# Optimization experiments

Measured on AMD Instinct MI355X. Metric: run time of the kernel, lower is better.

Reference implementation:

```python
import jax, jax.numpy as jnp
import numpy as np

N_USERS = 100000
N_ITEMS = 50000
N_ENT = 80000            # items + tags (tags = 30000)
N_NODES = N_USERS + N_ENT
N_EDGES = 800000
D = 64
N_LAYERS = 2


def _center_net(embs, idx, n, W1, b1, W2, b2):
    # CenterIntersection: linear+relu, linear, segment softmax, weighted segment sum
    act = jnp.maximum(embs @ W1.T + b1, 0.0)
    logits = act @ W2.T + b2
    m = jax.ops.segment_max(logits, idx, num_segments=n)
    e = jnp.exp(logits - m[idx])
    s = jax.ops.segment_sum(e, idx, num_segments=n)
    att = e / s[idx]
    return jax.ops.segment_sum(att * embs, idx, num_segments=n)


def _offset_net(embs, idx, mask, n, use_min, W1, b1, W2, b2):
    # BoxOffsetIntersection restricted to edges where mask is True
    mf = mask[:, None].astype(embs.dtype)
    act = jnp.maximum(embs @ W1.T + b1, 0.0) * mf
    cnt = jax.ops.segment_sum(mask.astype(embs.dtype), idx, num_segments=n)
    mean = jax.ops.segment_sum(act, idx, num_segments=n) / jnp.maximum(cnt, 1.0)[:, None]
    gate = jax.nn.sigmoid(mean @ W2.T + b2)
    if use_min:
        src = jnp.where(mask[:, None], embs, jnp.inf)
        red = jax.ops.segment_min(src, idx, num_segments=n)
    else:
        src = jnp.where(mask[:, None], embs, -jnp.inf)
        red = jax.ops.segment_max(src, idx, num_segments=n)
    red = jnp.where(jnp.isfinite(red), red, 0.0)  # torch_scatter fills empty segments with 0
    return red * gate


def setup_inputs() -> dict:
    key = jax.random.key(0)
    ks = jax.random.split(key, 10)
    s = 0.05  # xavier-like scale
    return {
        "user_emb": jax.random.normal(ks[0], (N_USERS, D), jnp.float32),
        "user_offset_emb": jax.random.normal(ks[1], (N_USERS, D), jnp.float32),
        "item_emb": jax.random.normal(ks[2], (N_ENT, D), jnp.float32),
        "item_offset_emb": jax.random.normal(ks[3], (N_ENT, D), jnp.float32),
        "cW1": jax.random.normal(ks[4], (D, D), jnp.float32) * s,
        "cb1": jnp.zeros((D,), jnp.float32),
        "cW2": jax.random.normal(ks[5], (D, D), jnp.float32) * s,
        "cb2": jnp.zeros((D,), jnp.float32),
        "oW1": jax.random.normal(ks[6], (D, D), jnp.float32) * s,
        "ob1": jnp.zeros((D,), jnp.float32),
        "oW2": jax.random.normal(ks[7], (D, D), jnp.float32) * s,
        "ob2": jnp.zeros((D,), jnp.float32),
        "head": jax.random.randint(ks[8], (N_EDGES,), 0, N_NODES, jnp.int32),
        "tail": jax.random.randint(ks[9], (N_EDGES,), 0, N_NODES, jnp.int32),
    }


def reference(user_emb, user_offset_emb, item_emb, item_offset_emb,
              cW1, cb1, cW2, cb2, oW1, ob1, oW2, ob2, head, tail):
    all_embs = jnp.concatenate([user_emb, item_emb], axis=0)              # [N_NODES, D]
    all_off = jnp.maximum(jnp.concatenate([user_offset_emb, item_offset_emb], axis=0), 0.0)
    uu_idx = jnp.concatenate([jnp.arange(N_USERS), jnp.arange(N_USERS)])
    uu_mask = jnp.ones((2 * N_USERS,), bool)
    m_inter = (tail >= N_USERS) & (head < N_USERS) & (tail < N_USERS + N_ITEMS)
    m_ut = (head < N_USERS) & (tail >= N_USERS + N_ITEMS)
    m_item = (head >= N_USERS) & (head < N_USERS + N_ITEMS)
    m_tag = head >= N_USERS + N_ITEMS
    for _ in range(N_LAYERS):
        h_embs = all_embs[tail]                                           # [E, D] gather
        agg_emb = _center_net(h_embs, head, N_NODES, cW1, cb1, cW2, cb2)
        edge_off = jnp.maximum(all_off[tail], 0.0)                        # [E, D]
        inter_u = _offset_net(edge_off, head, m_inter, N_NODES, True, oW1, ob1, oW2, ob2)[:N_USERS]
        ut_u = _offset_net(edge_off, head, m_ut, N_NODES, False, oW1, ob1, oW2, ob2)[:N_USERS]
        item_o = _offset_net(edge_off, head, m_item, N_NODES, False, oW1, ob1, oW2, ob2)[N_USERS:N_USERS + N_ITEMS]
        tag_o = _offset_net(edge_off, head, m_tag, N_NODES, True, oW1, ob1, oW2, ob2)[N_USERS + N_ITEMS:]
        uo_cat = jnp.concatenate([inter_u, ut_u], axis=0)                 # [2*N_USERS, D]
        user_o = jnp.maximum(_offset_net(uo_cat, uu_idx, uu_mask, N_USERS, False, oW1, ob1, oW2, ob2), 0.0)
        agg_off = jnp.concatenate([user_o, item_o, tag_o], axis=0)
        agg_emb = agg_emb / jnp.maximum(jnp.linalg.norm(agg_emb, axis=1, keepdims=True), 1e-12)  # F.normalize
        all_embs = agg_emb
        all_off = agg_off
    return (all_embs[:N_USERS], all_off[:N_USERS], all_embs[N_USERS:], all_off[N_USERS:])
```

## Files before the change

### kernel.cpp

```cpp
#include <hip/hip_runtime.h>
#include <hip/hip_fp16.h>
#include <math.h>

#define NU 100000
#define NI 50000
#define NENT 80000
#define NN 180000
#define NEDGE 800000
#define SCAN_NB ((NN + 1023) / 1024)

typedef _Float16 f16x4 __attribute__((ext_vector_type(4)));
typedef _Float16 f16x2 __attribute__((ext_vector_type(2)));
typedef float f32x4 __attribute__((ext_vector_type(4)));

__device__ __forceinline__ float sigmoid_f(float x) { return 1.0f / (1.0f + __expf(-x)); }
__device__ __forceinline__ unsigned pack2(float a, float b) {
    __half2 h = __floats2half2_rn(a, b);
    return *(unsigned*)&h;
}
__device__ __forceinline__ f16x2 u2h2(unsigned u) { union { unsigned u; f16x2 h; } x; x.u = u; return x.h; }
__device__ __forceinline__ float fdot2f(f16x2 a, f16x2 b, float c) {
#if __has_builtin(__builtin_amdgcn_fdot2)
    return __builtin_amdgcn_fdot2(a, b, c, false);
#else
    return (float)a[0] * (float)b[0] + (float)a[1] * (float)b[1] + c;
#endif
}
__device__ __forceinline__ _Float16 hminf(_Float16 a, _Float16 b) { return a < b ? a : b; }
__device__ __forceinline__ _Float16 hmaxf(_Float16 a, _Float16 b) { return a > b ? a : b; }
__device__ __forceinline__ f16x4 frag4(const float* __restrict__ p) {
    float4 v = *(const float4*)p;
    f16x4 r; r[0] = (_Float16)v.x; r[1] = (_Float16)v.y; r[2] = (_Float16)v.z; r[3] = (_Float16)v.w;
    return r;
}
__device__ __forceinline__ f16x4 frag4r(const float* __restrict__ p) {
    float4 v = *(const float4*)p;
    f16x4 r;
    r[0] = (_Float16)fmaxf(v.x, 0.f); r[1] = (_Float16)fmaxf(v.y, 0.f);
    r[2] = (_Float16)fmaxf(v.z, 0.f); r[3] = (_Float16)fmaxf(v.w, 0.f);
    return r;
}
__device__ __forceinline__ f16x4 fragp(const _Float16* __restrict__ Wp, int dt, int ks, int lane) {
    return *(const f16x4*)(Wp + (((dt * 4 + ks) * 64 + lane) << 2));
}
__device__ __forceinline__ f32x4 mm(f16x4 a, f16x4 b, f32x4 c) {
    return __builtin_amdgcn_mfma_f32_16x16x16f16(a, b, c, 0, 0, 0);
}

__global__ __launch_bounds__(256) void prep_w(
    const float* __restrict__ W0, const float* __restrict__ W1,
    const float* __restrict__ W2, const float* __restrict__ W3,
    _Float16* __restrict__ out)
{
    int idx = blockIdx.x * 256 + threadIdx.x;
    int mat = idx >> 12, wi = idx & 4095;
    const float* W = (mat == 0) ? W0 : (mat == 1) ? W1 : (mat == 2) ? W2 : W3;
    int tile = wi >> 8;
    int dt = tile >> 2, ks = tile & 3;
    int ln = (wi >> 2) & 63, j = wi & 3;
    int lr = ln & 15, lk = ln >> 4;
    out[idx] = (_Float16)W[(size_t)(dt * 16 + lr) * 64 + ks * 16 + lk * 4 + j];
}

__global__ __launch_bounds__(256) void node_pass(
    const float* __restrict__ embU, const float* __restrict__ embE,
    const float* __restrict__ offU, const float* __restrict__ offE,
    const _Float16* __restrict__ cW1f, const float* __restrict__ cb1,
    const _Float16* __restrict__ cW2f, const float* __restrict__ cb2,
    const _Float16* __restrict__ oW1f, const float* __restrict__ ob1,
    uint2* __restrict__ packed)
{
    __shared__ _Float16 tb[4][16 * 72];
    int lane = threadIdx.x & 63, wid = threadIdx.x >> 6;
    int n0 = (blockIdx.x * 4 + wid) * 16;
    if (n0 >= NN) return;
    int lr = lane & 15, lk = lane >> 4;
    const float* eb; const float* ob;
    if (n0 < NU) { eb = embU + (size_t)n0 * 64; ob = offU + (size_t)n0 * 64; }
    else         { eb = embE + (size_t)(n0 - NU) * 64; ob = offE + (size_t)(n0 - NU) * 64; }

    f16x4 ax[4];
    #pragma unroll
    for (int ks = 0; ks < 4; ++ks) ax[ks] = frag4(eb + (size_t)lr * 64 + ks * 16 + lk * 4);
    f32x4 acc[4];
    #pragma unroll
    for (int dt = 0; dt < 4; ++dt) {
        float b = cb1[dt * 16 + lr];
        f32x4 c = {b, b, b, b};
        #pragma unroll
        for (int ks = 0; ks < 4; ++ks) c = mm(ax[ks], fragp(cW1f, dt, ks, lane), c);
        acc[dt] = c;
    }
    _Float16* T = tb[wid];
    #pragma unroll
    for (int dt = 0; dt < 4; ++dt)
        #pragma unroll
        for (int r = 0; r < 4; ++r)
            T[(lk * 4 + r) * 72 + dt * 16 + lr] = (_Float16)fmaxf(acc[dt][r], 0.f);
    f16x4 a1[4];
    #pragma unroll
    for (int ks = 0; ks < 4; ++ks) a1[ks] = *(const f16x4*)(T + lr * 72 + ks * 16 + lk * 4);
    #pragma unroll
    for (int dt = 0; dt < 4; ++dt) {
        float b = cb2[dt * 16 + lr];
        f32x4 c = {b, b, b, b};
        #pragma unroll
        for (int ks = 0; ks < 4; ++ks) c = mm(a1[ks], fragp(cW2f, dt, ks, lane), c);
        acc[dt] = c;
    }
    f16x4 axo[4];
    #pragma unroll
    for (int ks = 0; ks < 4; ++ks) axo[ks] = frag4r(ob + (size_t)lr * 64 + ks * 16 + lk * 4);
    f32x4 acco[4];
    #pragma unroll
    for (int dt = 0; dt < 4; ++dt) {
        float b = ob1[dt * 16 + lr];
        f32x4 c = {b, b, b, b};
        #pragma unroll
        for (int ks = 0; ks < 4; ++ks) c = mm(axo[ks], fragp(oW1f, dt, ks, lane), c);
        acco[dt] = c;
    }
    #pragma unroll
    for (int ks = 0; ks < 4; ++ks) *(f16x4*)(T + lr * 72 + ks * 16 + lk * 4) = ax[ks];
    _Float16 xv[16];
    #pragma unroll
    for (int dt = 0; dt < 4; ++dt)
        #pragma unroll
        for (int r = 0; r < 4; ++r) xv[dt * 4 + r] = T[(lk * 4 + r) * 72 + dt * 16 + lr];
    #pragma unroll
    for (int ks = 0; ks < 4; ++ks) *(f16x4*)(T + lr * 72 + ks * 16 + lk * 4) = axo[ks];
    #pragma unroll
    for (int dt = 0; dt < 4; ++dt) {
        #pragma unroll
        for (int r = 0; r < 4; ++r) {
            int li = lk * 4 + r;
            float ev = __expf(acc[dt][r]);
            float xf = (float)xv[dt * 4 + r];
            float ovf = (float)T[(lk * 4 + r) * 72 + dt * 16 + lr];
            float aov = fmaxf(acco[dt][r], 0.f);
            packed[(size_t)(n0 + li) * 64 + dt * 16 + lr] = make_uint2(pack2(ev, ev * xf), pack2(aov, ovf));
        }
    }
}

__global__ __launch_bounds__(256) void hist_k(const int* __restrict__ head, int* __restrict__ counts) {
    int e = blockIdx.x * 256 + threadIdx.x;
    if (e < NEDGE) atomicAdd(&counts[head[e]], 1);
}

__global__ __launch_bounds__(1024) void scan_local(const int* __restrict__ counts,
                                                   int* __restrict__ excl, int* __restrict__ partials) {
    __shared__ int wsum[16];
    int tid = threadIdx.x, lane = tid & 63, wid = tid >> 6;
    int i = blockIdx.x * 1024 + tid;
    int v = (i < NN) ? counts[i] : 0;
    int s = v;
    #pragma unroll
    for (int d = 1; d < 64; d <<= 1) { int u = __shfl_up(s, d, 64); if (lane >= d) s += u; }
    if (lane == 63) wsum[wid] = s;
    __syncthreads();
    if (wid == 0 && lane < 16) {
        int w = wsum[lane];
        #pragma unroll
        for (int d = 1; d < 16; d <<= 1) { int u = __shfl_up(w, d, 64); if (lane >= d) w += u; }
        wsum[lane] = w;
    }
    __syncthreads();
    int base = wid ? wsum[wid - 1] : 0;
    if (i < NN) excl[i] = base + s - v;
    if (tid == 1023) partials[blockIdx.x] = wsum[15];
}

__global__ __launch_bounds__(256) void scan_carry(const int* __restrict__ partials, int* __restrict__ carries) {
    __shared__ int ws[4];
    int tid = threadIdx.x, lane = tid & 63, wid = tid >> 6;
    int v = (tid < SCAN_NB) ? partials[tid] : 0;
    int s = v;
    #pragma unroll
    for (int d = 1; d < 64; d <<= 1) { int u = __shfl_up(s, d, 64); if (lane >= d) s += u; }
    if (lane == 63) ws[wid] = s;
    __syncthreads();
    int add = 0;
    for (int w = 0; w < wid; ++w) add += ws[w];
    if (tid < SCAN_NB) carries[tid] = add + s - v;
}

__global__ __launch_bounds__(1024) void scan_add(int* __restrict__ excl, const int* __restrict__ carries,
                                                 int* __restrict__ cursor) {
    int i = blockIdx.x * 1024 + threadIdx.x;
    if (i < NN) { int o = excl[i] + carries[blockIdx.x]; excl[i] = o; cursor[i] = o; }
    if (i == 0) excl[NN] = NEDGE;
}

__global__ __launch_bounds__(256) void scatter_k(const int* __restrict__ head, const int* __restrict__ tail,
                                                 int* __restrict__ cursor, int* __restrict__ sorted_t) {
    int e = blockIdx.x * 256 + threadIdx.x;
    if (e < NEDGE) { int pos = atomicAdd(&cursor[head[e]], 1); sorted_t[pos] = tail[e]; }
}

__global__ __launch_bounds__(256) void seg_pass(
    const uint2* __restrict__ packed,
    const int* __restrict__ offsets, const int* __restrict__ sorted_t,
    float* __restrict__ embOutU, float* __restrict__ embOutE,
    _Float16* __restrict__ meanI, _Float16* __restrict__ redI,
    _Float16* __restrict__ meanU, _Float16* __restrict__ redU,
    _Float16* __restrict__ meanE, _Float16* __restrict__ redE)
{
    int lane = threadIdx.x & 63;
    int h = blockIdx.x * 4 + (threadIdx.x >> 6);
    int beg = offsets[h], end = offsets[h + 1];
    bool isUser = (h < NU);
    bool entMin = (h >= NU + NI);
    const f16x2 SEL_LO = {(_Float16)1.0f, (_Float16)0.0f};
    const f16x2 SEL_HI = {(_Float16)0.0f, (_Float16)1.0f};
    float num = 0.f, den = 0.f, s_i = 0.f, s_u = 0.f;
    const _Float16 HINF = u2h2(0x7C007C00u)[0];
    _Float16 m_i = (isUser || entMin) ? HINF : (_Float16)0.f;
    _Float16 m_u = (_Float16)0.f;
    int c_i = 0, c_u = 0;

    const char* pbase = (const char*)packed;
    int loff = lane << 3;
    for (int base = beg; base < end; base += 64) {
        int rem = end - base; if (rem > 64) rem = 64;
        int tv = sorted_t[base + (lane < rem ? lane : 0)];
        int t0 = __builtin_amdgcn_readlane(tv, 0);
        uint2 q0 = *(const uint2*)(pbase + ((size_t)(unsigned)t0 << 9) + loff);
        int t1 = t0; uint2 q1 = q0;
        if (rem > 1) {
            t1 = __builtin_amdgcn_readlane(tv, 1);
            q1 = *(const uint2*)(pbase + ((size_t)(unsigned)t1 << 9) + loff);
        }
        for (int j = 0; j < rem; ++j) {
            int tc = t0; uint2 qc = q0;
            t0 = t1; q0 = q1;
            if (j + 2 < rem) {
                t1 = __builtin_amdgcn_readlane(tv, j + 2);
                q1 = *(const uint2*)(pbase + ((size_t)(unsigned)t1 << 9) + loff);
            }
            f16x2 evp = u2h2(qc.x);
            den = fdot2f(evp, SEL_LO, den);
            num = fdot2f(evp, SEL_HI, num);
            f16x2 aoo = u2h2(qc.y);
            if (isUser) {
                if (tc >= NU) {
                    if (tc < NU + NI) { s_i = fdot2f(aoo, SEL_LO, s_i); m_i = hminf(m_i, aoo[1]); c_i++; }
                    else              { s_u = fdot2f(aoo, SEL_LO, s_u); m_u = hmaxf(m_u, aoo[1]); c_u++; }
                }
            } else {
                s_i = fdot2f(aoo, SEL_LO, s_i); c_i++;
                m_i = entMin ? hminf(m_i, aoo[1]) : hmaxf(m_i, aoo[1]);
            }
        }
    }
    float v = (den > 0.f) ? num / den : 0.f;
    float sq = v * v;
    #pragma unroll
    for (int m = 32; m; m >>= 1) sq += __shfl_xor(sq, m, 64);
    v = v / fmaxf(sqrtf(sq), 1e-12f);

    float m_if = (float)m_i;
    if (m_if > 1e37f) m_if = 0.f;
    float rc_i = __builtin_amdgcn_rcpf(fmaxf((float)c_i, 1.f));
    if (isUser) {
        embOutU[(size_t)h * 64 + lane] = v;
        size_t r = (size_t)h * 64 + lane;
        float rc_u = __builtin_amdgcn_rcpf(fmaxf((float)c_u, 1.f));
        meanI[r] = (_Float16)(s_i * rc_i);
        redI[r]  = (_Float16)m_if;
        meanU[r] = (_Float16)(s_u * rc_u);
        redU[r]  = m_u;
    } else {
        embOutE[(size_t)(h - NU) * 64 + lane] = v;
        size_t r = (size_t)(h - NU) * 64 + lane;
        meanE[r] = (_Float16)(s_i * rc_i);
        redE[r]  = (_Float16)m_if;
    }
}

__global__ __launch_bounds__(256) void ent_fin(
    const _Float16* __restrict__ meanE, const _Float16* __restrict__ redE,
    const _Float16* __restrict__ oW2f, const float* __restrict__ ob2,
    float* __restrict__ entOff)
{
    int lane = threadIdx.x & 63, wid = threadIdx.x >> 6;
    int n0 = (blockIdx.x * 4 + wid) * 16;
    if (n0 >= NENT) return;
    int lr = lane & 15, lk = lane >> 4;
    f16x4 am[4];
    #pragma unroll
    for (int ks = 0; ks < 4; ++ks) am[ks] = *(const f16x4*)(meanE + (size_t)(n0 + lr) * 64 + ks * 16 + lk * 4);
    #pragma unroll
    for (int dt = 0; dt < 4; ++dt) {
        float b = ob2[dt * 16 + lr];
        f32x4 c = {b, b, b, b};
        #pragma unroll
        for (int ks = 0; ks < 4; ++ks) c = mm(am[ks], fragp(oW2f, dt, ks, lane), c);
        #pragma unroll
        for (int r = 0; r < 4; ++r) {
            size_t row = (size_t)(n0 + lk * 4 + r);
            entOff[row * 64 + dt * 16 + lr] = (float)redE[row * 64 + dt * 16 + lr] * sigmoid_f(c[r]);
        }
    }
}

__global__ __launch_bounds__(256) void user_fin2(
    const _Float16* __restrict__ meanI, const _Float16* __restrict__ redI,
    const _Float16* __restrict__ meanU, const _Float16* __restrict__ redU,
    const _Float16* __restrict__ oW1f, const float* __restrict__ ob1,
    const _Float16* __restrict__ oW2f, const float* __restrict__ ob2,
    float* __restrict__ outOffU)
{
    __shared__ _Float16 tb[4][16 * 72];
    int lane = threadIdx.x & 63, wid = threadIdx.x >> 6;
    int u0 = (blockIdx.x * 4 + wid) * 16;
    if (u0 >= NU) return;
    int lr = lane & 15, lk = lane >> 4;
    _Float16* T = tb[wid];

    f16x4 W1f[4][4], W2f[4][4];
    float b1d[4], b2d[4];
    #pragma unroll
    for (int dt = 0; dt < 4; ++dt) {
        b1d[dt] = ob1[dt * 16 + lr]; b2d[dt] = ob2[dt * 16 + lr];
        #pragma unroll
        for (int ks = 0; ks < 4; ++ks) {
            W1f[dt][ks] = fragp(oW1f, dt, ks, lane);
            W2f[dt][ks] = fragp(oW2f, dt, ks, lane);
        }
    }

    f16x4 am[4];
    #pragma unroll
    for (int ks = 0; ks < 4; ++ks) am[ks] = *(const f16x4*)(meanI + (size_t)(u0 + lr) * 64 + ks * 16 + lk * 4);
    f32x4 iu[4], uu[4];
    #pragma unroll
    for (int dt = 0; dt < 4; ++dt) {
        f32x4 c = {b2d[dt], b2d[dt], b2d[dt], b2d[dt]};
        #pragma unroll
        for (int ks = 0; ks < 4; ++ks) c = mm(am[ks], W2f[dt][ks], c);
        #pragma unroll
        for (int r = 0; r < 4; ++r)
            iu[dt][r] = (float)redI[(size_t)(u0 + lk * 4 + r) * 64 + dt * 16 + lr] * sigmoid_f(c[r]);
    }
    #pragma unroll
    for (int ks = 0; ks < 4; ++ks) am[ks] = *(const f16x4*)(meanU + (size_t)(u0 + lr) * 64 + ks * 16 + lk * 4);
    #pragma unroll
    for (int dt = 0; dt < 4; ++dt) {
        f32x4 c = {b2d[dt], b2d[dt], b2d[dt], b2d[dt]};
        #pragma unroll
        for (int ks = 0; ks < 4; ++ks) c = mm(am[ks], W2f[dt][ks], c);
        #pragma unroll
        for (int r = 0; r < 4; ++r)
            uu[dt][r] = (float)redU[(size_t)(u0 + lk * 4 + r) * 64 + dt * 16 + lr] * sigmoid_f(c[r]);
    }
    #pragma unroll
    for (int dt = 0; dt < 4; ++dt)
        #pragma unroll
        for (int r = 0; r < 4; ++r) T[(lk * 4 + r) * 72 + dt * 16 + lr] = (_Float16)iu[dt][r];
    #pragma unroll
    for (int ks = 0; ks < 4; ++ks) am[ks] = *(const f16x4*)(T + lr * 72 + ks * 16 + lk * 4);
    f32x4 mn[4];
    #pragma unroll
    for (int dt = 0; dt < 4; ++dt) {
        f32x4 c = {b1d[dt], b1d[dt], b1d[dt], b1d[dt]};
        #pragma unroll
        for (int ks = 0; ks < 4; ++ks) c = mm(am[ks], W1f[dt][ks], c);
        #pragma unroll
        for (int r = 0; r < 4; ++r) mn[dt][r] = fmaxf(c[r], 0.f);
    }
    #pragma unroll
    for (int dt = 0; dt < 4; ++dt)
        #pragma unroll
        for (int r = 0; r < 4; ++r) T[(lk * 4 + r) * 72 + dt * 16 + lr] = (_Float16)uu[dt][r];
    #pragma unroll
    for (int ks = 0; ks < 4; ++ks) am[ks] = *(const f16x4*)(T + lr * 72 + ks * 16 + lk * 4);
    #pragma unroll
    for (int dt = 0; dt < 4; ++dt) {
        f32x4 c = {b1d[dt], b1d[dt], b1d[dt], b1d[dt]};
        #pragma unroll
        for (int ks = 0; ks < 4; ++ks) c = mm(am[ks], W1f[dt][ks], c);
        #pragma unroll
        for (int r = 0; r < 4; ++r) mn[dt][r] = 0.5f * (mn[dt][r] + fmaxf(c[r], 0.f));
    }
    #pragma unroll
    for (int dt = 0; dt < 4; ++dt)
        #pragma unroll
        for (int r = 0; r < 4; ++r) T[(lk * 4 + r) * 72 + dt * 16 + lr] = (_Float16)mn[dt][r];
    #pragma unroll
    for (int ks = 0; ks < 4; ++ks) am[ks] = *(const f16x4*)(T + lr * 72 + ks * 16 + lk * 4);
    #pragma unroll
    for (int dt = 0; dt < 4; ++dt) {
        f32x4 c = {b2d[dt], b2d[dt], b2d[dt], b2d[dt]};
        #pragma unroll
        for (int ks = 0; ks < 4; ++ks) c = mm(am[ks], W2f[dt][ks], c);
        #pragma unroll
        for (int r = 0; r < 4; ++r)
            outOffU[(size_t)(u0 + lk * 4 + r) * 64 + dt * 16 + lr] =
                fmaxf(fmaxf(iu[dt][r], uu[dt][r]) * sigmoid_f(c[r]), 0.f);
    }
}

extern "C" void kernel_launch(void* const* d_in, const int* in_sizes, int n_in,
                              void* d_out, int out_size, void* d_ws, size_t ws_size,
                              hipStream_t stream)
{
    const float* user_emb = (const float*)d_in[0];
    const float* user_off = (const float*)d_in[1];
    const float* item_emb = (const float*)d_in[2];
    const float* item_off = (const float*)d_in[3];
    const float* cW1 = (const float*)d_in[4];
    const float* cb1 = (const float*)d_in[5];
    const float* cW2 = (const float*)d_in[6];
    const float* cb2 = (const float*)d_in[7];
    const float* oW1 = (const float*)d_in[8];
    const float* ob1 = (const float*)d_in[9];
    const float* oW2 = (const float*)d_in[10];
    const float* ob2 = (const float*)d_in[11];
    const int* head = (const int*)d_in[12];
    const int* tail = (const int*)d_in[13];
    float* out = (float*)d_out;

    float* ws = (float*)d_ws;
    const size_t SZ = (size_t)NN * 64;
    float* A      = ws;
    float* B      = A + SZ;
    uint2* packed = (uint2*)(B + SZ);
    _Float16* meanI_h = (_Float16*)(packed + SZ);
    _Float16* redI_h  = meanI_h + (size_t)NU * 64;
    _Float16* meanU_h = redI_h + (size_t)NU * 64;
    _Float16* redU_h  = meanU_h + (size_t)NU * 64;
    _Float16* meanE_h = redU_h + (size_t)NU * 64;
    _Float16* redE_h  = meanE_h + (size_t)NENT * 64;
    _Float16* wpre    = redE_h + (size_t)NENT * 64;
    int* counts   = (int*)(wpre + 4 * 4096);
    int* offsets  = counts + NN;
    int* cursor   = offsets + NN + 1;
    int* sorted_t = cursor + NN;
    int* partials = sorted_t + NEDGE;
    int* carries  = partials + SCAN_NB;

    const _Float16* cW1f = wpre;
    const _Float16* cW2f = wpre + 4096;
    const _Float16* oW1f = wpre + 8192;
    const _Float16* oW2f = wpre + 12288;

    prep_w<<<64, 256, 0, stream>>>(cW1, cW2, oW1, oW2, wpre);
    hipMemsetAsync(counts, 0, NN * sizeof(int), stream);
    hist_k<<<(NEDGE + 255) / 256, 256, 0, stream>>>(head, counts);
    scan_local<<<SCAN_NB, 1024, 0, stream>>>(counts, offsets, partials);
    scan_carry<<<1, 256, 0, stream>>>(partials, carries);
    scan_add<<<SCAN_NB, 1024, 0, stream>>>(offsets, carries, cursor);
    scatter_k<<<(NEDGE + 255) / 256, 256, 0, stream>>>(head, tail, cursor, sorted_t);

    for (int layer = 0; layer < 2; ++layer) {
        const float *eU, *eE, *oU, *oE;
        float *embOutU, *embOutE, *entOff, *uOffOut;
        if (layer == 0) {
            eU = user_emb; eE = item_emb; oU = user_off; oE = item_off;
            embOutU = A;               embOutE = A + (size_t)NU * 64;
            entOff  = B + (size_t)NU * 64;
            uOffOut = B;
        } else {
            eU = A; eE = A + (size_t)NU * 64; oU = B; oE = B + (size_t)NU * 64;
            embOutU = out;             embOutE = out + (size_t)2 * NU * 64;
            entOff  = out + ((size_t)2 * NU + NENT) * 64;
            uOffOut = out + (size_t)NU * 64;
        }
        node_pass<<<(NN + 63) / 64, 256, 0, stream>>>(eU, eE, oU, oE,
                                                      cW1f, cb1, cW2f, cb2, oW1f, ob1, packed);
        seg_pass<<<NN / 4, 256, 0, stream>>>(packed, offsets, sorted_t,
                                             embOutU, embOutE,
                                             meanI_h, redI_h, meanU_h, redU_h,
                                             meanE_h, redE_h);
        ent_fin<<<(NENT / 16 + 3) / 4, 256, 0, stream>>>(meanE_h, redE_h, oW2f, ob2, entOff);
        user_fin2<<<(NU + 63) / 64, 256, 0, stream>>>(meanI_h, redI_h, meanU_h, redU_h,
                                                      oW1f, ob1, oW2f, ob2, uOffOut);
    }
}
```

Measured before the change: 444.5 us.

## Store layer-1 intermediates in fp16 and split packed edge data into two arrays

Layer-1 embeddings and offsets are now written to and read from the workspace as fp16 instead of fp32, which halves the traffic between the two layers. The packed per-node payload is split into separate softmax and offset arrays. In seg_pass, user segments then load the offset half only for neighbours that are entities, so neighbours that are users skip the second load. The cost is one extra fp16 rounding of the intermediate embeddings and two narrower gathers in place of one 8-byte gather.

```diff
diff --git a/kernel.cpp b/kernel.cpp
--- a/kernel.cpp
+++ b/kernel.cpp
@@ -28,17 +28,31 @@
 }
 __device__ __forceinline__ _Float16 hminf(_Float16 a, _Float16 b) { return a < b ? a : b; }
 __device__ __forceinline__ _Float16 hmaxf(_Float16 a, _Float16 b) { return a > b ? a : b; }
-__device__ __forceinline__ f16x4 frag4(const float* __restrict__ p) {
-    float4 v = *(const float4*)p;
-    f16x4 r; r[0] = (_Float16)v.x; r[1] = (_Float16)v.y; r[2] = (_Float16)v.z; r[3] = (_Float16)v.w;
-    return r;
-}
-__device__ __forceinline__ f16x4 frag4r(const float* __restrict__ p) {
-    float4 v = *(const float4*)p;
-    f16x4 r;
-    r[0] = (_Float16)fmaxf(v.x, 0.f); r[1] = (_Float16)fmaxf(v.y, 0.f);
-    r[2] = (_Float16)fmaxf(v.z, 0.f); r[3] = (_Float16)fmaxf(v.w, 0.f);
-    return r;
+
+template<typename T>
+__device__ __forceinline__ f16x4 ldfrag(const T* __restrict__ p) {
+    if constexpr (sizeof(T) == 2) {
+        return *(const f16x4*)p;
+    } else {
+        float4 v = *(const float4*)p;
+        f16x4 r; r[0] = (_Float16)v.x; r[1] = (_Float16)v.y; r[2] = (_Float16)v.z; r[3] = (_Float16)v.w;
+        return r;
+    }
+}
+template<typename T>
+__device__ __forceinline__ f16x4 ldfragr(const T* __restrict__ p) {
+    if constexpr (sizeof(T) == 2) {
+        f16x4 v = *(const f16x4*)p;
+        #pragma unroll
+        for (int i = 0; i < 4; ++i) v[i] = hmaxf(v[i], (_Float16)0.f);
+        return v;
+    } else {
+        float4 v = *(const float4*)p;
+        f16x4 r;
+        r[0] = (_Float16)fmaxf(v.x, 0.f); r[1] = (_Float16)fmaxf(v.y, 0.f);
+        r[2] = (_Float16)fmaxf(v.z, 0.f); r[3] = (_Float16)fmaxf(v.w, 0.f);
+        return r;
+    }
 }
 __device__ __forceinline__ f16x4 fragp(const _Float16* __restrict__ Wp, int dt, int ks, int lane) {
     return *(const f16x4*)(Wp + (((dt * 4 + ks) * 64 + lane) << 2));
@@ -62,26 +76,27 @@
     out[idx] = (_Float16)W[(size_t)(dt * 16 + lr) * 64 + ks * 16 + lk * 4 + j];
 }
 
+template<typename T>
 __global__ __launch_bounds__(256) void node_pass(
-    const float* __restrict__ embU, const float* __restrict__ embE,
-    const float* __restrict__ offU, const float* __restrict__ offE,
+    const T* __restrict__ embU, const T* __restrict__ embE,
+    const T* __restrict__ offU, const T* __restrict__ offE,
     const _Float16* __restrict__ cW1f, const float* __restrict__ cb1,
     const _Float16* __restrict__ cW2f, const float* __restrict__ cb2,
     const _Float16* __restrict__ oW1f, const float* __restrict__ ob1,
-    uint2* __restrict__ packed)
+    unsigned* __restrict__ packedA, unsigned* __restrict__ packedB)
 {
     __shared__ _Float16 tb[4][16 * 72];
     int lane = threadIdx.x & 63, wid = threadIdx.x >> 6;
     int n0 = (blockIdx.x * 4 + wid) * 16;
     if (n0 >= NN) return;
     int lr = lane & 15, lk = lane >> 4;
-    const float* eb; const float* ob;
+    const T* eb; const T* ob;
     if (n0 < NU) { eb = embU + (size_t)n0 * 64; ob = offU + (size_t)n0 * 64; }
     else         { eb = embE + (size_t)(n0 - NU) * 64; ob = offE + (size_t)(n0 - NU) * 64; }
 
     f16x4 ax[4];
     #pragma unroll
-    for (int ks = 0; ks < 4; ++ks) ax[ks] = frag4(eb + (size_t)lr * 64 + ks * 16 + lk * 4);
+    for (int ks = 0; ks < 4; ++ks) ax[ks] = ldfrag(eb + (size_t)lr * 64 + ks * 16 + lk * 4);
     f32x4 acc[4];
     #pragma unroll
     for (int dt = 0; dt < 4; ++dt) {
@@ -91,15 +106,15 @@
         for (int ks = 0; ks < 4; ++ks) c = mm(ax[ks], fragp(cW1f, dt, ks, lane), c);
         acc[dt] = c;
     }
-    _Float16* T = tb[wid];
+    _Float16* T16 = tb[wid];
     #pragma unroll
     for (int dt = 0; dt < 4; ++dt)
         #pragma unroll
         for (int r = 0; r < 4; ++r)
-            T[(lk * 4 + r) * 72 + dt * 16 + lr] = (_Float16)fmaxf(acc[dt][r], 0.f);
+            T16[(lk * 4 + r) * 72 + dt * 16 + lr] = (_Float16)fmaxf(acc[dt][r], 0.f);
     f16x4 a1[4];
     #pragma unroll
-    for (int ks = 0; ks < 4; ++ks) a1[ks] = *(const f16x4*)(T + lr * 72 + ks * 16 + lk * 4);
+    for (int ks = 0; ks < 4; ++ks) a1[ks] = *(const f16x4*)(T16 + lr * 72 + ks * 16 + lk * 4);
     #pragma unroll
     for (int dt = 0; dt < 4; ++dt) {
         float b = cb2[dt * 16 + lr];
@@ -110,7 +125,7 @@
     }
     f16x4 axo[4];
     #pragma unroll
-    for (int ks = 0; ks < 4; ++ks) axo[ks] = frag4r(ob + (size_t)lr * 64 + ks * 16 + lk * 4);
+    for (int ks = 0; ks < 4; ++ks) axo[ks] = ldfragr(ob + (size_t)lr * 64 + ks * 16 + lk * 4);
     f32x4 acco[4];
     #pragma unroll
     for (int dt = 0; dt < 4; ++dt) {
@@ -121,14 +136,14 @@
         acco[dt] = c;
     }
     #pragma unroll
-    for (int ks = 0; ks < 4; ++ks) *(f16x4*)(T + lr * 72 + ks * 16 + lk * 4) = ax[ks];
+    for (int ks = 0; ks < 4; ++ks) *(f16x4*)(T16 + lr * 72 + ks * 16 + lk * 4) = ax[ks];
     _Float16 xv[16];
     #pragma unroll
     for (int dt = 0; dt < 4; ++dt)
         #pragma unroll
-        for (int r = 0; r < 4; ++r) xv[dt * 4 + r] = T[(lk * 4 + r) * 72 + dt * 16 + lr];
-    #pragma unroll
-    for (int ks = 0; ks < 4; ++ks) *(f16x4*)(T + lr * 72 + ks * 16 + lk * 4) = axo[ks];
+        for (int r = 0; r < 4; ++r) xv[dt * 4 + r] = T16[(lk * 4 + r) * 72 + dt * 16 + lr];
+    #pragma unroll
+    for (int ks = 0; ks < 4; ++ks) *(f16x4*)(T16 + lr * 72 + ks * 16 + lk * 4) = axo[ks];
     #pragma unroll
     for (int dt = 0; dt < 4; ++dt) {
         #pragma unroll
@@ -136,9 +151,11 @@
             int li = lk * 4 + r;
             float ev = __expf(acc[dt][r]);
             float xf = (float)xv[dt * 4 + r];
-            float ovf = (float)T[(lk * 4 + r) * 72 + dt * 16 + lr];
+            float ovf = (float)T16[(lk * 4 + r) * 72 + dt * 16 + lr];
             float aov = fmaxf(acco[dt][r], 0.f);
-            packed[(size_t)(n0 + li) * 64 + dt * 16 + lr] = make_uint2(pack2(ev, ev * xf), pack2(aov, ovf));
+            size_t idx = (size_t)(n0 + li) * 64 + dt * 16 + lr;
+            packedA[idx] = pack2(ev, ev * xf);
+            packedB[idx] = pack2(aov, ovf);
         }
     }
 }
@@ -198,10 +215,11 @@
     if (e < NEDGE) { int pos = atomicAdd(&cursor[head[e]], 1); sorted_t[pos] = tail[e]; }
 }
 
+template<bool OUT16>
 __global__ __launch_bounds__(256) void seg_pass(
-    const uint2* __restrict__ packed,
+    const unsigned* __restrict__ packedA, const unsigned* __restrict__ packedB,
     const int* __restrict__ offsets, const int* __restrict__ sorted_t,
-    float* __restrict__ embOutU, float* __restrict__ embOutE,
+    void* __restrict__ embOutU_, void* __restrict__ embOutE_,
     _Float16* __restrict__ meanI, _Float16* __restrict__ redI,
     _Float16* __restrict__ meanU, _Float16* __restrict__ redU,
     _Float16* __restrict__ meanE, _Float16* __restrict__ redE)
@@ -219,37 +237,43 @@
     _Float16 m_u = (_Float16)0.f;
     int c_i = 0, c_u = 0;
 
-    const char* pbase = (const char*)packed;
-    int loff = lane << 3;
+    const char* pA = (const char*)packedA;
+    const char* pB = (const char*)packedB;
+    int loff = lane << 2;
     for (int base = beg; base < end; base += 64) {
         int rem = end - base; if (rem > 64) rem = 64;
         int tv = sorted_t[base + (lane < rem ? lane : 0)];
         int t0 = __builtin_amdgcn_readlane(tv, 0);
-        uint2 q0 = *(const uint2*)(pbase + ((size_t)(unsigned)t0 << 9) + loff);
-        int t1 = t0; uint2 q1 = q0;
+        unsigned a0 = *(const unsigned*)(pA + ((size_t)(unsigned)t0 << 8) + loff);
+        unsigned b0 = 0;
+        if (!isUser || t0 >= NU) b0 = *(const unsigned*)(pB + ((size_t)(unsigned)t0 << 8) + loff);
+        int t1 = t0; unsigned a1 = a0, b1 = b0;
         if (rem > 1) {
             t1 = __builtin_amdgcn_readlane(tv, 1);
-            q1 = *(const uint2*)(pbase + ((size_t)(unsigned)t1 << 9) + loff);
+            a1 = *(const unsigned*)(pA + ((size_t)(unsigned)t1 << 8) + loff);
+            if (!isUser || t1 >= NU) b1 = *(const unsigned*)(pB + ((size_t)(unsigned)t1 << 8) + loff);
         }
         for (int j = 0; j < rem; ++j) {
-            int tc = t0; uint2 qc = q0;
-            t0 = t1; q0 = q1;
+            int tc = t0; unsigned qa = a0, qb = b0;
+            t0 = t1; a0 = a1; b0 = b1;
             if (j + 2 < rem) {
                 t1 = __builtin_amdgcn_readlane(tv, j + 2);
-                q1 = *(const uint2*)(pbase + ((size_t)(unsigned)t1 << 9) + loff);
+                a1 = *(const unsigned*)(pA + ((size_t)(unsigned)t1 << 8) + loff);
+                if (!isUser || t1 >= NU) b1 = *(const unsigned*)(pB + ((size_t)(unsigned)t1 << 8) + loff);
             }
-            f16x2 evp = u2h2(qc.x);
-            den = fdot2f(evp, SEL_LO, den);
-            num = fdot2f(evp, SEL_HI, num);
-            f16x2 aoo = u2h2(qc.y);
+            f16x2 ea = u2h2(qa);
+            den = fdot2f(ea, SEL_LO, den);
+            num = fdot2f(ea, SEL_HI, num);
             if (isUser) {
                 if (tc >= NU) {
-                    if (tc < NU + NI) { s_i = fdot2f(aoo, SEL_LO, s_i); m_i = hminf(m_i, aoo[1]); c_i++; }
-                    else              { s_u = fdot2f(aoo, SEL_LO, s_u); m_u = hmaxf(m_u, aoo[1]); c_u++; }
+                    f16x2 ab = u2h2(qb);
+                    if (tc < NU + NI) { s_i = fdot2f(ab, SEL_LO, s_i); m_i = hminf(m_i, ab[1]); c_i++; }
+                    else              { s_u = fdot2f(ab, SEL_LO, s_u); m_u = hmaxf(m_u, ab[1]); c_u++; }
                 }
             } else {
-                s_i = fdot2f(aoo, SEL_LO, s_i); c_i++;
-                m_i = entMin ? hminf(m_i, aoo[1]) : hmaxf(m_i, aoo[1]);
+                f16x2 ab = u2h2(qb);
+                s_i = fdot2f(ab, SEL_LO, s_i); c_i++;
+                m_i = entMin ? hminf(m_i, ab[1]) : hmaxf(m_i, ab[1]);
             }
         }
     }
@@ -263,25 +287,28 @@
     if (m_if > 1e37f) m_if = 0.f;
     float rc_i = __builtin_amdgcn_rcpf(fmaxf((float)c_i, 1.f));
     if (isUser) {
-        embOutU[(size_t)h * 64 + lane] = v;
         size_t r = (size_t)h * 64 + lane;
+        if constexpr (OUT16) ((_Float16*)embOutU_)[r] = (_Float16)v;
+        else                 ((float*)embOutU_)[r] = v;
         float rc_u = __builtin_amdgcn_rcpf(fmaxf((float)c_u, 1.f));
         meanI[r] = (_Float16)(s_i * rc_i);
         redI[r]  = (_Float16)m_if;
         meanU[r] = (_Float16)(s_u * rc_u);
         redU[r]  = m_u;
     } else {
-        embOutE[(size_t)(h - NU) * 64 + lane] = v;
         size_t r = (size_t)(h - NU) * 64 + lane;
+        if constexpr (OUT16) ((_Float16*)embOutE_)[r] = (_Float16)v;
+        else                 ((float*)embOutE_)[r] = v;
         meanE[r] = (_Float16)(s_i * rc_i);
         redE[r]  = (_Float16)m_if;
     }
 }
 
+template<bool OUT16>
 __global__ __launch_bounds__(256) void ent_fin(
     const _Float16* __restrict__ meanE, const _Float16* __restrict__ redE,
     const _Float16* __restrict__ oW2f, const float* __restrict__ ob2,
-    float* __restrict__ entOff)
+    void* __restrict__ entOff_)
 {
     int lane = threadIdx.x & 63, wid = threadIdx.x >> 6;
     int n0 = (blockIdx.x * 4 + wid) * 16;
@@ -299,24 +326,27 @@
         #pragma unroll
         for (int r = 0; r < 4; ++r) {
             size_t row = (size_t)(n0 + lk * 4 + r);
-            entOff[row * 64 + dt * 16 + lr] = (float)redE[row * 64 + dt * 16 + lr] * sigmoid_f(c[r]);
+            float val = (float)redE[row * 64 + dt * 16 + lr] * sigmoid_f(c[r]);
+            if constexpr (OUT16) ((_Float16*)entOff_)[row * 64 + dt * 16 + lr] = (_Float16)val;
+            else                 ((float*)entOff_)[row * 64 + dt * 16 + lr] = val;
         }
     }
 }
 
+template<bool OUT16>
 __global__ __launch_bounds__(256) void user_fin2(
     const _Float16* __restrict__ meanI, const _Float16* __restrict__ redI,
     const _Float16* __restrict__ meanU, const _Float16* __restrict__ redU,
     const _Float16* __restrict__ oW1f, const float* __restrict__ ob1,
     const _Float16* __restrict__ oW2f, const float* __restrict__ ob2,
-    float* __restrict__ outOffU)
+    void* __restrict__ outOffU_)
 {
     __shared__ _Float16 tb[4][16 * 72];
     int lane = threadIdx.x & 63, wid = threadIdx.x >> 6;
     int u0 = (blockIdx.x * 4 + wid) * 16;
     if (u0 >= NU) return;
     int lr = lane & 15, lk = lane >> 4;
-    _Float16* T = tb[wid];
+    _Float16* T16 = tb[wid];
 
     f16x4 W1f[4][4], W2f[4][4];
     float b1d[4], b2d[4];
@@ -357,9 +387,9 @@
     #pragma unroll
     for (int dt = 0; dt < 4; ++dt)
         #pragma unroll
-        for (int r = 0; r < 4; ++r) T[(lk * 4 + r) * 72 + dt * 16 + lr] = (_Float16)iu[dt][r];
-    #pragma unroll
-    for (int ks = 0; ks < 4; ++ks) am[ks] = *(const f16x4*)(T + lr * 72 + ks * 16 + lk * 4);
+        for (int r = 0; r < 4; ++r) T16[(lk * 4 + r) * 72 + dt * 16 + lr] = (_Float16)iu[dt][r];
+    #pragma unroll
+    for (int ks = 0; ks < 4; ++ks) am[ks] = *(const f16x4*)(T16 + lr * 72 + ks * 16 + lk * 4);
     f32x4 mn[4];
     #pragma unroll
     for (int dt = 0; dt < 4; ++dt) {
@@ -372,9 +402,9 @@
     #pragma unroll
     for (int dt = 0; dt < 4; ++dt)
         #pragma unroll
-        for (int r = 0; r < 4; ++r) T[(lk * 4 + r) * 72 + dt * 16 + lr] = (_Float16)uu[dt][r];
-    #pragma unroll
-    for (int ks = 0; ks < 4; ++ks) am[ks] = *(const f16x4*)(T + lr * 72 + ks * 16 + lk * 4);
+        for (int r = 0; r < 4; ++r) T16[(lk * 4 + r) * 72 + dt * 16 + lr] = (_Float16)uu[dt][r];
+    #pragma unroll
+    for (int ks = 0; ks < 4; ++ks) am[ks] = *(const f16x4*)(T16 + lr * 72 + ks * 16 + lk * 4);
     #pragma unroll
     for (int dt = 0; dt < 4; ++dt) {
         f32x4 c = {b1d[dt], b1d[dt], b1d[dt], b1d[dt]};
@@ -386,18 +416,21 @@
     #pragma unroll
     for (int dt = 0; dt < 4; ++dt)
         #pragma unroll
-        for (int r = 0; r < 4; ++r) T[(lk * 4 + r) * 72 + dt * 16 + lr] = (_Float16)mn[dt][r];
-    #pragma unroll
-    for (int ks = 0; ks < 4; ++ks) am[ks] = *(const f16x4*)(T + lr * 72 + ks * 16 + lk * 4);
+        for (int r = 0; r < 4; ++r) T16[(lk * 4 + r) * 72 + dt * 16 + lr] = (_Float16)mn[dt][r];
+    #pragma unroll
+    for (int ks = 0; ks < 4; ++ks) am[ks] = *(const f16x4*)(T16 + lr * 72 + ks * 16 + lk * 4);
     #pragma unroll
     for (int dt = 0; dt < 4; ++dt) {
         f32x4 c = {b2d[dt], b2d[dt], b2d[dt], b2d[dt]};
         #pragma unroll
         for (int ks = 0; ks < 4; ++ks) c = mm(am[ks], W2f[dt][ks], c);
         #pragma unroll
-        for (int r = 0; r < 4; ++r)
-            outOffU[(size_t)(u0 + lk * 4 + r) * 64 + dt * 16 + lr] =
-                fmaxf(fmaxf(iu[dt][r], uu[dt][r]) * sigmoid_f(c[r]), 0.f);
+        for (int r = 0; r < 4; ++r) {
+            float val = fmaxf(fmaxf(iu[dt][r], uu[dt][r]) * sigmoid_f(c[r]), 0.f);
+            size_t idx = (size_t)(u0 + lk * 4 + r) * 64 + dt * 16 + lr;
+            if constexpr (OUT16) ((_Float16*)outOffU_)[idx] = (_Float16)val;
+            else                 ((float*)outOffU_)[idx] = val;
+        }
     }
 }
 
@@ -421,12 +454,12 @@
     const int* tail = (const int*)d_in[13];
     float* out = (float*)d_out;
 
-    float* ws = (float*)d_ws;
     const size_t SZ = (size_t)NN * 64;
-    float* A      = ws;
-    float* B      = A + SZ;
-    uint2* packed = (uint2*)(B + SZ);
-    _Float16* meanI_h = (_Float16*)(packed + SZ);
+    _Float16* A16   = (_Float16*)d_ws;
+    _Float16* B16   = A16 + SZ;
+    unsigned* packedA = (unsigned*)(B16 + SZ);
+    unsigned* packedB = packedA + SZ;
+    _Float16* meanI_h = (_Float16*)(packedB + SZ);
     _Float16* redI_h  = meanI_h + (size_t)NU * 64;
     _Float16* meanU_h = redI_h + (size_t)NU * 64;
     _Float16* redU_h  = meanU_h + (size_t)NU * 64;
@@ -453,28 +486,27 @@
     scan_add<<<SCAN_NB, 1024, 0, stream>>>(offsets, carries, cursor);
     scatter_k<<<(NEDGE + 255) / 256, 256, 0, stream>>>(head, tail, cursor, sorted_t);
 
-    for (int layer = 0; layer < 2; ++layer) {
-        const float *eU, *eE, *oU, *oE;
-        float *embOutU, *embOutE, *entOff, *uOffOut;
-        if (layer == 0) {
-            eU = user_emb; eE = item_emb; oU = user_off; oE = item_off;
-            embOutU = A;               embOutE = A + (size_t)NU * 64;
-            entOff  = B + (size_t)NU * 64;
-            uOffOut = B;
-        } else {
-            eU = A; eE = A + (size_t)NU * 64; oU = B; oE = B + (size_t)NU * 64;
-            embOutU = out;             embOutE = out + (size_t)2 * NU * 64;
-            entOff  = out + ((size_t)2 * NU + NENT) * 64;
-            uOffOut = out + (size_t)NU * 64;
-        }
-        node_pass<<<(NN + 63) / 64, 256, 0, stream>>>(eU, eE, oU, oE,
-                                                      cW1f, cb1, cW2f, cb2, oW1f, ob1, packed);
-        seg_pass<<<NN / 4, 256, 0, stream>>>(packed, offsets, sorted_t,
-                                             embOutU, embOutE,
-                                             meanI_h, redI_h, meanU_h, redU_h,
-                                             meanE_h, redE_h);
-        ent_fin<<<(NENT / 16 + 3) / 4, 256, 0, stream>>>(meanE_h, redE_h, oW2f, ob2, entOff);
-        user_fin2<<<(NU + 63) / 64, 256, 0, stream>>>(meanI_h, redI_h, meanU_h, redU_h,
-                                                      oW1f, ob1, oW2f, ob2, uOffOut);
-    }
-}
+    node_pass<float><<<(NN + 63) / 64, 256, 0, stream>>>(
+        user_emb, item_emb, user_off, item_off,
+        cW1f, cb1, cW2f, cb2, oW1f, ob1, packedA, packedB);
+    seg_pass<true><<<NN / 4, 256, 0, stream>>>(
+        packedA, packedB, offsets, sorted_t,
+        A16, A16 + (size_t)NU * 64,
+        meanI_h, redI_h, meanU_h, redU_h, meanE_h, redE_h);
+    ent_fin<true><<<(NENT / 16 + 3) / 4, 256, 0, stream>>>(
+        meanE_h, redE_h, oW2f, ob2, B16 + (size_t)NU * 64);
+    user_fin2<true><<<(NU + 63) / 64, 256, 0, stream>>>(
+        meanI_h, redI_h, meanU_h, redU_h, oW1f, ob1, oW2f, ob2, B16);
+
+    node_pass<_Float16><<<(NN + 63) / 64, 256, 0, stream>>>(
+        A16, A16 + (size_t)NU * 64, B16, B16 + (size_t)NU * 64,
+        cW1f, cb1, cW2f, cb2, oW1f, ob1, packedA, packedB);
+    seg_pass<false><<<NN / 4, 256, 0, stream>>>(
+        packedA, packedB, offsets, sorted_t,
+        out, out + (size_t)2 * NU * 64,
+        meanI_h, redI_h, meanU_h, redU_h, meanE_h, redE_h);
+    ent_fin<false><<<(NENT / 16 + 3) / 4, 256, 0, stream>>>(
+        meanE_h, redE_h, oW2f, ob2, out + ((size_t)2 * NU + NENT) * 64);
+    user_fin2<false><<<(NU + 63) / 64, 256, 0, stream>>>(
+        meanI_h, redI_h, meanU_h, redU_h, oW1f, ob1, oW2f, ob2, out + (size_t)NU * 64);
+}
```

Result: no change. 436.2 us (-1.9%).
